# Optimization experiments

Measured on AMD Instinct MI355X. Metric: run time of the kernel, lower is better.

Reference implementation:

```python
import jax, jax.numpy as jnp
import numpy as np

B, S, D, H = 2, 2048, 1024, 16
DK = D // H
SOFTCAP = 30.0


def setup_inputs() -> dict:
    key = jax.random.key(0)
    ks = jax.random.split(key, 6)
    inp = jax.random.normal(ks[0], (B, S, D), dtype=jnp.float32)
    count_bias = jax.random.normal(ks[1], (B, 1, S, S), dtype=jnp.float32) * 0.1
    # causal boolean mask: True = allowed
    causal = jnp.tril(jnp.ones((S, S), dtype=bool))
    attn_mask = jnp.broadcast_to(causal[None, None, :, :], (B, 1, S, S))
    scale = 0.02
    Wq = jax.random.normal(ks[2], (D, D), dtype=jnp.float32) * scale
    Wk = jax.random.normal(ks[3], (D, D), dtype=jnp.float32) * scale
    Wv = jax.random.normal(ks[4], (D, D), dtype=jnp.float32) * scale
    Wo = jax.random.normal(ks[5], (D, D), dtype=jnp.float32) * scale
    return {"inp": inp, "count_bias": count_bias, "attn_mask": attn_mask,
            "Wq": Wq, "Wk": Wk, "Wv": Wv, "Wo": Wo}


def reference(inp, count_bias, attn_mask, Wq, Wk, Wv, Wo):
    b = inp.shape[0]
    # nn.Linear: y = x @ W.T ; reshape to (B, H, S, DK)
    def proj(x, W):
        return jnp.einsum('bsd,ed->bse', x, W).reshape(b, -1, H, DK).transpose(0, 2, 1, 3)
    q = proj(inp, Wq)
    k = proj(inp, Wk)
    v = proj(inp, Wv)
    scale = 1.0 / np.sqrt(DK).astype(np.float32)
    scores = jnp.einsum('bhqd,bhkd->bhqk', q, k) * scale  # (B,H,S,S)
    scores = scores + count_bias  # broadcast over heads
    scores = jnp.tanh(scores / SOFTCAP) * SOFTCAP  # softcap > 0
    scores = jnp.where(attn_mask, scores, -jnp.inf)
    weights = jax.nn.softmax(scores, axis=-1)
    o = jnp.einsum('bhqk,bhkd->bhqd', weights, v)
    o = o.transpose(0, 2, 1, 3).reshape(b, -1, D)
    out = jnp.einsum('bsd,ed->bse', o, Wo)
    return out
```

## Files before the change

kernel.cpp:

```cpp
#include <hip/hip_runtime.h>
#include <hip/hip_bf16.h>

#define GK 1024

typedef __attribute__((ext_vector_type(8))) short bf16x8;
typedef __attribute__((ext_vector_type(4))) float f32x4;
typedef __attribute__((ext_vector_type(16))) float f32x16;
typedef __attribute__((ext_vector_type(4))) unsigned short ushort4v;

__device__ __forceinline__ f32x4 mfma16(bf16x8 a, bf16x8 b, f32x4 c) {
  return __builtin_amdgcn_mfma_f32_16x16x32_bf16(a, b, c, 0, 0, 0);
}
__device__ __forceinline__ f32x16 mfma32(bf16x8 a, bf16x8 b, f32x16 c) {
  return __builtin_amdgcn_mfma_f32_32x32x16_bf16(a, b, c, 0, 0, 0);
}

__device__ __forceinline__ unsigned short f2b(float f) {
  union { float f; unsigned int u; } x; x.f = f;
  return (unsigned short)((x.u + 0x7fffu + ((x.u >> 16) & 1u)) >> 16);
}

__device__ __forceinline__ unsigned int pk2(float lo, float hi) {
  float2 f; f.x = lo; f.y = hi;
  __hip_bfloat162 t = __float22bfloat162_rn(f);
  union { __hip_bfloat162 b; unsigned int u; } c; c.b = t;
  return c.u;
}

__device__ __forceinline__ float fexp2(float x) {
#if __has_builtin(__builtin_amdgcn_exp2f)
  return __builtin_amdgcn_exp2f(x);
#else
  return exp2f(x);
#endif
}
__device__ __forceinline__ float frcp(float x) {
#if __has_builtin(__builtin_amdgcn_rcpf)
  return __builtin_amdgcn_rcpf(x);
#else
  return 1.0f / x;
#endif
}

__global__ __launch_bounds__(256) void convert_kernel(
    const float* __restrict__ inp,
    const float* __restrict__ wq, const float* __restrict__ wk,
    const float* __restrict__ wv, const float* __restrict__ wo,
    unsigned short* __restrict__ Xb, unsigned short* __restrict__ Wcat)
{
  const size_t XN = (size_t)4194304;
  size_t i = ((size_t)blockIdx.x * 256 + threadIdx.x) * 4;
  const float* src; unsigned short* dst; size_t off;
  if (i < XN) {
    src = inp; dst = Xb; off = i;
  } else {
    size_t j = i - XN;
    int w = (int)(j >> 20);
    off = j & 1048575u;
    src = (w == 0) ? wq : (w == 1) ? wk : (w == 2) ? wv : wo;
    dst = Wcat + ((size_t)w << 20);
  }
  f32x4 v = *(const f32x4*)(src + off);
  ushort4v o;
#pragma unroll
  for (int t = 0; t < 4; ++t) o[t] = f2b(v[t]);
  *(ushort4v*)(dst + off) = o;
}

__device__ __forceinline__ void gemm_mainloop(
    const unsigned short* __restrict__ A, const unsigned short* __restrict__ Wt,
    int m0, int n0, int tid, unsigned short* As, unsigned short* Bs,
    f32x4 (&acc)[4][4])
{
  const int lane = tid & 63;
  const int wave = tid >> 6;
  const int wr = wave >> 1, wc = wave & 1;
  const int lq = lane & 15, g = lane >> 4;
  const int srow = tid >> 2;
  const int scol = (tid & 3) * 8;

  const unsigned short* Ap = A + (size_t)(m0 + srow) * GK + scol;
  const unsigned short* Wp = Wt + (size_t)(n0 + srow) * GK + scol;

  for (int kt = 0; kt < GK / 32; ++kt) {
    const int k0 = kt * 32;
    uint4 a0 = *(const uint4*)(Ap + k0);
    uint4 a1 = *(const uint4*)(Ap + (size_t)64 * GK + k0);
    uint4 b0 = *(const uint4*)(Wp + k0);
    uint4 b1 = *(const uint4*)(Wp + (size_t)64 * GK + k0);
    __syncthreads();
    *(uint4*)(As + srow * 32 + scol) = a0;
    *(uint4*)(As + (64 + srow) * 32 + scol) = a1;
    *(uint4*)(Bs + srow * 32 + scol) = b0;
    *(uint4*)(Bs + (64 + srow) * 32 + scol) = b1;
    __syncthreads();
    bf16x8 af[4], bfr[4];
#pragma unroll
    for (int i = 0; i < 4; ++i)
      af[i] = *(const bf16x8*)(As + (wr * 64 + i * 16 + lq) * 32 + g * 8);
#pragma unroll
    for (int j = 0; j < 4; ++j)
      bfr[j] = *(const bf16x8*)(Bs + (wc * 64 + j * 16 + lq) * 32 + g * 8);
#pragma unroll
    for (int i = 0; i < 4; ++i)
#pragma unroll
      for (int j = 0; j < 4; ++j)
        acc[i][j] = mfma16(af[i], bfr[j], acc[i][j]);
  }
}

__global__ __launch_bounds__(256) void gemm_qkv(
    const unsigned short* __restrict__ X, const unsigned short* __restrict__ Wcat,
    unsigned short* __restrict__ Qb, unsigned short* __restrict__ Kb,
    unsigned short* __restrict__ Vt)
{
  __shared__ unsigned short As[4096];
  __shared__ unsigned short Bs[4096];
  f32x4 acc[4][4];
#pragma unroll
  for (int i = 0; i < 4; ++i)
#pragma unroll
    for (int j = 0; j < 4; ++j) acc[i][j] = (f32x4){0.f, 0.f, 0.f, 0.f};

  const int z = blockIdx.z;
  const int m0 = blockIdx.x * 128, n0 = blockIdx.y * 128;
  gemm_mainloop(X, Wcat + ((size_t)z << 20), m0, n0, (int)threadIdx.x, As, Bs, acc);

  const int lane = threadIdx.x & 63;
  const int wave = threadIdx.x >> 6;
  const int wr = wave >> 1, wc = wave & 1, lq = lane & 15, g = lane >> 4;

  if (z < 2) {
    unsigned short* C = z ? Kb : Qb;
#pragma unroll
    for (int i = 0; i < 4; ++i)
#pragma unroll
      for (int j = 0; j < 4; ++j) {
        int col = n0 + wc * 64 + j * 16 + lq;
#pragma unroll
        for (int r = 0; r < 4; ++r) {
          int row = m0 + wr * 64 + i * 16 + g * 4 + r;
          C[(size_t)row * 1024 + col] = f2b(acc[i][j][r]);
        }
      }
  } else {
#pragma unroll
    for (int i = 0; i < 4; ++i)
#pragma unroll
      for (int j = 0; j < 4; ++j) {
        int col = n0 + wc * 64 + j * 16 + lq;
        int row0 = m0 + wr * 64 + i * 16 + g * 4;
        int b = row0 >> 11;
        int s = row0 & 2047;
        ushort4v pv;
#pragma unroll
        for (int r = 0; r < 4; ++r) pv[r] = f2b(acc[i][j][r]);
        *(ushort4v*)(Vt + (size_t)(b * 1024 + col) * 2048 + s) = pv;
      }
  }
}

__global__ __launch_bounds__(256) void gemm_out(
    const unsigned short* __restrict__ Ob, const unsigned short* __restrict__ Wo,
    float* __restrict__ out)
{
  __shared__ unsigned short As[4096];
  __shared__ unsigned short Bs[4096];
  f32x4 acc[4][4];
#pragma unroll
  for (int i = 0; i < 4; ++i)
#pragma unroll
    for (int j = 0; j < 4; ++j) acc[i][j] = (f32x4){0.f, 0.f, 0.f, 0.f};

  const int m0 = blockIdx.x * 128, n0 = blockIdx.y * 128;
  gemm_mainloop(Ob, Wo, m0, n0, (int)threadIdx.x, As, Bs, acc);

  const int lane = threadIdx.x & 63;
  const int wave = threadIdx.x >> 6;
  const int wr = wave >> 1, wc = wave & 1, lq = lane & 15, g = lane >> 4;
#pragma unroll
  for (int i = 0; i < 4; ++i)
#pragma unroll
    for (int j = 0; j < 4; ++j) {
      int col = n0 + wc * 64 + j * 16 + lq;
#pragma unroll
      for (int r = 0; r < 4; ++r) {
        int row = m0 + wr * 64 + i * 16 + g * 4 + r;
        out[(size_t)row * 1024 + col] = acc[i][j][r];
      }
    }
}

__device__ __forceinline__ void attn_chain(
    const bf16x8 (&qf)[4], const f32x4 (&bvs)[4],
    bf16x8 kf0, bf16x8 kf1, bf16x8 kf2, bf16x8 kf3,
    bf16x8 va00, bf16x8 va01, bf16x8 va10, bf16x8 va11,
    bool msk, int ql, int hi,
    f32x16& o0, f32x16& o1, float& pls)
{
  const float INV30 = 0.033333333333f;
  const float C3 = -0.333333333f, C5 = 0.133333333f;
  const float C1 = 43.28085122666891f;

  f32x16 st = {0.f,0.f,0.f,0.f,0.f,0.f,0.f,0.f,0.f,0.f,0.f,0.f,0.f,0.f,0.f,0.f};
  st = mfma32(kf0, qf[0], st);
  st = mfma32(kf1, qf[1], st);
  st = mfma32(kf2, qf[2], st);
  st = mfma32(kf3, qf[3], st);

  float p[16];
#pragma unroll
  for (int reg = 0; reg < 16; ++reg) {
    float v = fmaf(st[reg], 0.125f, bvs[reg >> 2][reg & 3]);
    float y = v * INV30;
    float y2 = y * y;
    float t = y * fmaf(y2, fmaf(y2, C5, C3), 1.0f);
    p[reg] = fexp2(fmaf(t, C1, -C1));
  }
  if (msk) {
#pragma unroll
    for (int reg = 0; reg < 16; ++reg) {
      int krow = (reg & 3) + 8 * (reg >> 2) + 4 * hi;
      p[reg] = (krow <= ql) ? p[reg] : 0.f;
    }
  }
  float a0 = (p[0] + p[1]) + (p[2] + p[3]);
  float a1 = (p[4] + p[5]) + (p[6] + p[7]);
  float a2 = (p[8] + p[9]) + (p[10] + p[11]);
  float a3 = (p[12] + p[13]) + (p[14] + p[15]);
  pls += (a0 + a1) + (a2 + a3);

  unsigned int wv[8];
#pragma unroll
  for (int j = 0; j < 8; ++j) wv[j] = pk2(p[2 * j], p[2 * j + 1]);
  unsigned int x0 = hi ? wv[0] : wv[2], x1 = hi ? wv[1] : wv[3];
  x0 = __shfl_xor(x0, 32); x1 = __shfl_xor(x1, 32);
  unsigned int y0 = hi ? wv[4] : wv[6], y1 = hi ? wv[5] : wv[7];
  y0 = __shfl_xor(y0, 32); y1 = __shfl_xor(y1, 32);
  union { unsigned int u[4]; bf16x8 v; } B0, B1;
  B0.u[0] = hi ? x0 : wv[0]; B0.u[1] = hi ? x1 : wv[1];
  B0.u[2] = hi ? wv[2] : x0; B0.u[3] = hi ? wv[3] : x1;
  B1.u[0] = hi ? y0 : wv[4]; B1.u[1] = hi ? y1 : wv[5];
  B1.u[2] = hi ? wv[6] : y0; B1.u[3] = hi ? wv[7] : y1;

  o0 = mfma32(va00, B0.v, o0);
  o0 = mfma32(va01, B1.v, o0);
  o1 = mfma32(va10, B0.v, o1);
  o1 = mfma32(va11, B1.v, o1);
}

__global__ __launch_bounds__(256, 2) void attn_fwd(
    const unsigned short* __restrict__ Qb, const unsigned short* __restrict__ Kb,
    const unsigned short* __restrict__ Vt, const float* __restrict__ bias,
    unsigned short* __restrict__ Ob)
{
  __shared__ float Obuf[2][2][64 * 33];
  __shared__ float lsumbuf[2][8 * 32];
  __shared__ float rowinv[2][32];

  const int lane = threadIdx.x & 63;
  const int w = threadIdx.x >> 6;
  const int qp = 31 - (blockIdx.x >> 5);
  const int bh = blockIdx.x & 31;
  const int b = bh >> 4, h = bh & 15;
  const int tA = 2 * qp, tB = 2 * qp + 1;
  const int q0A = tA * 32;
  const int ql = lane & 31;
  const int hi = lane >> 5;

  const unsigned short* QpA = Qb + (size_t)(b * 2048 + q0A + ql) * 1024 + h * 64 + 8 * hi;
  bf16x8 qfA[4], qfB[4];
#pragma unroll
  for (int c = 0; c < 4; ++c) {
    qfA[c] = *(const bf16x8*)(QpA + 16 * c);
    qfB[c] = *(const bf16x8*)(QpA + 32 * 1024 + 16 * c);
  }

  const unsigned short* Kp = Kb + (size_t)(b * 2048 + ql) * 1024 + h * 64 + 8 * hi;
  const unsigned short* Vp = Vt + (size_t)(bh * 64 + ql) * 2048 + 8 * hi;
  const float* BpA = bias + (size_t)b * 2048 * 2048 + (size_t)(q0A + ql) * 2048 + 4 * hi;
  const float* BpB = BpA + (size_t)32 * 2048;

  float plsA = 0.f, plsB = 0.f;
  f32x16 oA0 = {0.f,0.f,0.f,0.f,0.f,0.f,0.f,0.f,0.f,0.f,0.f,0.f,0.f,0.f,0.f,0.f};
  f32x16 oA1 = oA0, oB0 = oA0, oB1 = oA0;

  int kt = w;
  for (; kt <= tA; kt += 4) {
    const int k0 = kt * 32;
    const unsigned short* kp = Kp + (size_t)k0 * 1024;
    bf16x8 kf0 = *(const bf16x8*)(kp);
    bf16x8 kf1 = *(const bf16x8*)(kp + 16);
    bf16x8 kf2 = *(const bf16x8*)(kp + 32);
    bf16x8 kf3 = *(const bf16x8*)(kp + 48);
    const unsigned short* vp = Vp + k0;
    bf16x8 va00 = *(const bf16x8*)(vp);
    bf16x8 va01 = *(const bf16x8*)(vp + 16);
    bf16x8 va10 = *(const bf16x8*)(vp + (size_t)32 * 2048);
    bf16x8 va11 = *(const bf16x8*)(vp + (size_t)32 * 2048 + 16);
    f32x4 bvsA[4], bvsB[4];
#pragma unroll
    for (int j = 0; j < 4; ++j) {
      bvsA[j] = *(const f32x4*)(BpA + k0 + 8 * j);
      bvsB[j] = *(const f32x4*)(BpB + k0 + 8 * j);
    }
    attn_chain(qfA, bvsA, kf0, kf1, kf2, kf3, va00, va01, va10, va11,
               kt == tA, ql, hi, oA0, oA1, plsA);
    attn_chain(qfB, bvsB, kf0, kf1, kf2, kf3, va00, va01, va10, va11,
               false, ql, hi, oB0, oB1, plsB);
  }
  if (kt == tB) {
    const int k0 = tB * 32;
    const unsigned short* kp = Kp + (size_t)k0 * 1024;
    bf16x8 kf0 = *(const bf16x8*)(kp);
    bf16x8 kf1 = *(const bf16x8*)(kp + 16);
    bf16x8 kf2 = *(const bf16x8*)(kp + 32);
    bf16x8 kf3 = *(const bf16x8*)(kp + 48);
    const unsigned short* vp = Vp + k0;
    bf16x8 va00 = *(const bf16x8*)(vp);
    bf16x8 va01 = *(const bf16x8*)(vp + 16);
    bf16x8 va10 = *(const bf16x8*)(vp + (size_t)32 * 2048);
    bf16x8 va11 = *(const bf16x8*)(vp + (size_t)32 * 2048 + 16);
    f32x4 bvsB[4];
#pragma unroll
    for (int j = 0; j < 4; ++j) bvsB[j] = *(const f32x4*)(BpB + k0 + 8 * j);
    attn_chain(qfB, bvsB, kf0, kf1, kf2, kf3, va00, va01, va10, va11,
               true, ql, hi, oB0, oB1, plsB);
  }

  lsumbuf[0][(w * 2 + hi) * 32 + ql] = plsA;
  lsumbuf[1][(w * 2 + hi) * 32 + ql] = plsB;
  if (w >= 2) {
#pragma unroll
    for (int reg = 0; reg < 16; ++reg) {
      int d0 = (reg & 3) + 8 * (reg >> 2) + 4 * hi;
      Obuf[0][w - 2][d0 * 33 + ql] = oA0[reg];
      Obuf[0][w - 2][(d0 + 32) * 33 + ql] = oA1[reg];
      Obuf[1][w - 2][d0 * 33 + ql] = oB0[reg];
      Obuf[1][w - 2][(d0 + 32) * 33 + ql] = oB1[reg];
    }
  }
  __syncthreads();
  if (w < 2) {
#pragma unroll
    for (int reg = 0; reg < 16; ++reg) {
      int d0 = (reg & 3) + 8 * (reg >> 2) + 4 * hi;
      Obuf[0][w][d0 * 33 + ql] += oA0[reg];
      Obuf[0][w][(d0 + 32) * 33 + ql] += oA1[reg];
      Obuf[1][w][d0 * 33 + ql] += oB0[reg];
      Obuf[1][w][(d0 + 32) * 33 + ql] += oB1[reg];
    }
  }
  __syncthreads();
  if (threadIdx.x < 64) {
    int t = threadIdx.x >> 5, q = threadIdx.x & 31;
    float s = 0.f;
#pragma unroll
    for (int j = 0; j < 8; ++j) s += lsumbuf[t][j * 32 + q];
    rowinv[t][q] = frcp(s);
  }
  __syncthreads();
#pragma unroll
  for (int it = 0; it < 16; ++it) {
    int i = it * 256 + (int)threadIdx.x;
    int t = i >> 11;
    int rem = i & 2047;
    int q = rem >> 6, d = rem & 63;
    float val = (Obuf[t][0][d * 33 + q] + Obuf[t][1][d * 33 + q]) * rowinv[t][q];
    int row = b * 2048 + q0A + t * 32 + q;
    Ob[(size_t)row * 1024 + h * 64 + d] = f2b(val);
  }
}

extern "C" void kernel_launch(void* const* d_in, const int* in_sizes, int n_in,
                              void* d_out, int out_size, void* d_ws, size_t ws_size,
                              hipStream_t stream) {
  (void)in_sizes; (void)n_in; (void)out_size; (void)ws_size;
  const float* inp  = (const float*)d_in[0];
  const float* bias = (const float*)d_in[1];
  const float* wq = (const float*)d_in[3];
  const float* wk = (const float*)d_in[4];
  const float* wv = (const float*)d_in[5];
  const float* wo = (const float*)d_in[6];
  float* out = (float*)d_out;

  unsigned short* Xb   = (unsigned short*)d_ws;
  unsigned short* Wcat = Xb + 4194304;
  unsigned short* Qb   = Wcat + 4194304;
  unsigned short* Kb   = Qb + 4194304;
  unsigned short* Vt   = Kb + 4194304;
  unsigned short* Ob   = Vt + 4194304;

  convert_kernel<<<8192, 256, 0, stream>>>(inp, wq, wk, wv, wo, Xb, Wcat);
  gemm_qkv<<<dim3(32, 8, 3), dim3(256), 0, stream>>>(Xb, Wcat, Qb, Kb, Vt);
  attn_fwd<<<1024, 256, 0, stream>>>(Qb, Kb, Vt, bias, Ob);
  gemm_out<<<dim3(32, 8, 1), dim3(256), 0, stream>>>(Ob, Wcat + 3 * 1048576, out);
}
```

Measured before the change: 155.4 us.

## Balance causal attention work by pairing tiles, use direct global-to-LDS loads in GEMM

Result: slower. 167.5 us (+7.8%).

```diff
diff --git a/kernel.cpp b/kernel.cpp
--- a/kernel.cpp
+++ b/kernel.cpp
@@ -40,6 +40,12 @@
 #else
   return 1.0f / x;
 #endif
+}
+
+__device__ __forceinline__ void gl_lds16(const unsigned short* g, unsigned short* l) {
+  __builtin_amdgcn_global_load_lds(
+      (const __attribute__((address_space(1))) unsigned int*)g,
+      (__attribute__((address_space(3))) unsigned int*)l, 16, 0, 0);
 }
 
 __global__ __launch_bounds__(256) void convert_kernel(
@@ -76,23 +82,24 @@
   const int wave = tid >> 6;
   const int wr = wave >> 1, wc = wave & 1;
   const int lq = lane & 15, g = lane >> 4;
-  const int srow = tid >> 2;
-  const int scol = (tid & 3) * 8;
-
-  const unsigned short* Ap = A + (size_t)(m0 + srow) * GK + scol;
-  const unsigned short* Wp = Wt + (size_t)(n0 + srow) * GK + scol;
+
+  const int r_in = lane >> 2;
+  const int c8 = (lane & 3) * 8;
+
+  const unsigned short* Ap0 = A + (size_t)(m0 + wave * 32 + r_in) * GK + c8;
+  const unsigned short* Ap1 = Ap0 + (size_t)16 * GK;
+  const unsigned short* Wp0 = Wt + (size_t)(n0 + wave * 32 + r_in) * GK + c8;
+  const unsigned short* Wp1 = Wp0 + (size_t)16 * GK;
+  unsigned short* As0 = As + wave * 1024;
+  unsigned short* Bs0 = Bs + wave * 1024;
 
   for (int kt = 0; kt < GK / 32; ++kt) {
     const int k0 = kt * 32;
-    uint4 a0 = *(const uint4*)(Ap + k0);
-    uint4 a1 = *(const uint4*)(Ap + (size_t)64 * GK + k0);
-    uint4 b0 = *(const uint4*)(Wp + k0);
-    uint4 b1 = *(const uint4*)(Wp + (size_t)64 * GK + k0);
     __syncthreads();
-    *(uint4*)(As + srow * 32 + scol) = a0;
-    *(uint4*)(As + (64 + srow) * 32 + scol) = a1;
-    *(uint4*)(Bs + srow * 32 + scol) = b0;
-    *(uint4*)(Bs + (64 + srow) * 32 + scol) = b1;
+    gl_lds16(Ap0 + k0, As0);
+    gl_lds16(Ap1 + k0, As0 + 512);
+    gl_lds16(Wp0 + k0, Bs0);
+    gl_lds16(Wp1 + k0, Bs0 + 512);
     __syncthreads();
     bf16x8 af[4], bfr[4];
 #pragma unroll
@@ -260,33 +267,35 @@
 
   const int lane = threadIdx.x & 63;
   const int w = threadIdx.x >> 6;
-  const int qp = 31 - (blockIdx.x >> 5);
-  const int bh = blockIdx.x & 31;
+  const int bid = blockIdx.x;
+  const int lwg = (bid & 7) * 128 + (bid >> 3);
+  const int bh = lwg >> 5;
+  const int qp = lwg & 31;
   const int b = bh >> 4, h = bh & 15;
-  const int tA = 2 * qp, tB = 2 * qp + 1;
-  const int q0A = tA * 32;
+  const int tA = qp, tB = 63 - qp;
+  const int q0A = tA * 32, q0B = tB * 32;
   const int ql = lane & 31;
   const int hi = lane >> 5;
 
   const unsigned short* QpA = Qb + (size_t)(b * 2048 + q0A + ql) * 1024 + h * 64 + 8 * hi;
+  const unsigned short* QpB = Qb + (size_t)(b * 2048 + q0B + ql) * 1024 + h * 64 + 8 * hi;
   bf16x8 qfA[4], qfB[4];
 #pragma unroll
   for (int c = 0; c < 4; ++c) {
     qfA[c] = *(const bf16x8*)(QpA + 16 * c);
-    qfB[c] = *(const bf16x8*)(QpA + 32 * 1024 + 16 * c);
+    qfB[c] = *(const bf16x8*)(QpB + 16 * c);
   }
 
   const unsigned short* Kp = Kb + (size_t)(b * 2048 + ql) * 1024 + h * 64 + 8 * hi;
   const unsigned short* Vp = Vt + (size_t)(bh * 64 + ql) * 2048 + 8 * hi;
-  const float* BpA = bias + (size_t)b * 2048 * 2048 + (size_t)(q0A + ql) * 2048 + 4 * hi;
-  const float* BpB = BpA + (size_t)32 * 2048;
+  const float* BpA = bias + (size_t)b * 4194304 + (size_t)(q0A + ql) * 2048 + 4 * hi;
+  const float* BpB = bias + (size_t)b * 4194304 + (size_t)(q0B + ql) * 2048 + 4 * hi;
 
   float plsA = 0.f, plsB = 0.f;
   f32x16 oA0 = {0.f,0.f,0.f,0.f,0.f,0.f,0.f,0.f,0.f,0.f,0.f,0.f,0.f,0.f,0.f,0.f};
   f32x16 oA1 = oA0, oB0 = oA0, oB1 = oA0;
 
-  int kt = w;
-  for (; kt <= tA; kt += 4) {
+  for (int kt = w; kt <= tB; kt += 4) {
     const int k0 = kt * 32;
     const unsigned short* kp = Kp + (size_t)k0 * 1024;
     bf16x8 kf0 = *(const bf16x8*)(kp);
@@ -298,34 +307,18 @@
     bf16x8 va01 = *(const bf16x8*)(vp + 16);
     bf16x8 va10 = *(const bf16x8*)(vp + (size_t)32 * 2048);
     bf16x8 va11 = *(const bf16x8*)(vp + (size_t)32 * 2048 + 16);
-    f32x4 bvsA[4], bvsB[4];
-#pragma unroll
-    for (int j = 0; j < 4; ++j) {
-      bvsA[j] = *(const f32x4*)(BpA + k0 + 8 * j);
-      bvsB[j] = *(const f32x4*)(BpB + k0 + 8 * j);
-    }
-    attn_chain(qfA, bvsA, kf0, kf1, kf2, kf3, va00, va01, va10, va11,
-               kt == tA, ql, hi, oA0, oA1, plsA);
+    f32x4 bvsB[4];
+#pragma unroll
+    for (int j = 0; j < 4; ++j) bvsB[j] = *(const f32x4*)(BpB + k0 + 8 * j);
+    if (kt <= tA) {
+      f32x4 bvsA[4];
+#pragma unroll
+      for (int j = 0; j < 4; ++j) bvsA[j] = *(const f32x4*)(BpA + k0 + 8 * j);
+      attn_chain(qfA, bvsA, kf0, kf1, kf2, kf3, va00, va01, va10, va11,
+                 kt == tA, ql, hi, oA0, oA1, plsA);
+    }
     attn_chain(qfB, bvsB, kf0, kf1, kf2, kf3, va00, va01, va10, va11,
-               false, ql, hi, oB0, oB1, plsB);
-  }
-  if (kt == tB) {
-    const int k0 = tB * 32;
-    const unsigned short* kp = Kp + (size_t)k0 * 1024;
-    bf16x8 kf0 = *(const bf16x8*)(kp);
-    bf16x8 kf1 = *(const bf16x8*)(kp + 16);
-    bf16x8 kf2 = *(const bf16x8*)(kp + 32);
-    bf16x8 kf3 = *(const bf16x8*)(kp + 48);
-    const unsigned short* vp = Vp + k0;
-    bf16x8 va00 = *(const bf16x8*)(vp);
-    bf16x8 va01 = *(const bf16x8*)(vp + 16);
-    bf16x8 va10 = *(const bf16x8*)(vp + (size_t)32 * 2048);
-    bf16x8 va11 = *(const bf16x8*)(vp + (size_t)32 * 2048 + 16);
-    f32x4 bvsB[4];
-#pragma unroll
-    for (int j = 0; j < 4; ++j) bvsB[j] = *(const f32x4*)(BpB + k0 + 8 * j);
-    attn_chain(qfB, bvsB, kf0, kf1, kf2, kf3, va00, va01, va10, va11,
-               true, ql, hi, oB0, oB1, plsB);
+               kt == tB, ql, hi, oB0, oB1, plsB);
   }
 
   lsumbuf[0][(w * 2 + hi) * 32 + ql] = plsA;
@@ -367,7 +360,7 @@
     int rem = i & 2047;
     int q = rem >> 6, d = rem & 63;
     float val = (Obuf[t][0][d * 33 + q] + Obuf[t][1][d * 33 + q]) * rowinv[t][q];
-    int row = b * 2048 + q0A + t * 32 + q;
+    int row = b * 2048 + (t ? q0B : q0A) + q;
     Ob[(size_t)row * 1024 + h * 64 + d] = f2b(val);
   }
 }
```
